# Kernel optimization log

Measured on AMD Instinct MI355X. Metric: run time of the kernel, lower is better.

## Reference

```python
import jax, jax.numpy as jnp
import numpy as np

NUM_HEAD = 16
EMB_DIM = 1024
HEAD_DIM = EMB_DIM // NUM_HEAD

def setup_inputs() -> dict:
    key = jax.random.key(0)
    ks = jax.random.split(key, 9)
    B, S, D = 2, 2048, EMB_DIM
    s = 1.0 / np.sqrt(D)
    return {
        "x": jax.random.normal(ks[0], (B, S, D), dtype=jnp.float32),
        "Wq": jax.random.normal(ks[1], (D, D), dtype=jnp.float32) * s,
        "bq": jnp.zeros((D,), dtype=jnp.float32),
        "Wk": jax.random.normal(ks[2], (D, D), dtype=jnp.float32) * s,
        "bk": jnp.zeros((D,), dtype=jnp.float32),
        "Wv": jax.random.normal(ks[3], (D, D), dtype=jnp.float32) * s,
        "bv": jnp.zeros((D,), dtype=jnp.float32),
        "Wo": jax.random.normal(ks[4], (D, D), dtype=jnp.float32) * s,
        "bo": jnp.zeros((D,), dtype=jnp.float32),
    }

def reference(x, Wq, bq, Wk, bk, Wv, bv, Wo, bo):
    B, S, D = x.shape
    H, Hd = NUM_HEAD, HEAD_DIM
    # projections (torch Linear: x @ W.T + b; here W stored as [in, out])
    Q = (x @ Wq + bq).reshape(B, S, H, Hd)
    K = (x @ Wk + bk).reshape(B, S, H, Hd)
    V = (x @ Wv + bv).reshape(B, S, H, Hd)
    scale = jnp.sqrt(jnp.asarray(Hd, dtype=x.dtype))
    scores = jnp.einsum('bqhd,bkhd->bhqk', Q, K) / scale  # [B,H,S,S]
    attn = jax.nn.softmax(scores, axis=-1)
    out = jnp.einsum('bhql,blhd->bqhd', attn, V).reshape(B, S, D)
    return out @ Wo + bo
```

## Files before the change

### kernel.cpp

```cpp
#include <hip/hip_runtime.h>
#include <math.h>


using bf16   = __bf16;
using bf16x8 = __attribute__((ext_vector_type(8))) __bf16;
using bf16x4 = __attribute__((ext_vector_type(4))) __bf16;
using f32x4  = __attribute__((ext_vector_type(4))) float;

#define MFMA16(a, b, c) __builtin_amdgcn_mfma_f32_16x16x32_bf16((a), (b), (c), 0, 0, 0)
#define WAIT_VM0() asm volatile("s_waitcnt vmcnt(0)" ::: "memory")
#define WAITBAR(N) asm volatile("s_waitcnt vmcnt(" #N ")\n\ts_barrier" ::: "memory")

__device__ __forceinline__ bf16x8 ld8(const bf16* p) { return *(const bf16x8*)p; }

__device__ __forceinline__ void ldg_lds16(bf16* lds_base, const bf16* g) {
    __builtin_amdgcn_global_load_lds(
        (const __attribute__((address_space(1))) void*)g,
        (__attribute__((address_space(3))) void*)lds_base, 16, 0, 0);
}

__device__ __forceinline__ float fast_exp2(float x) {
#if __has_builtin(__builtin_amdgcn_exp2f)
    return __builtin_amdgcn_exp2f(x);
#else
    return exp2f(x);
#endif
}

__global__ __launch_bounds__(256) void prep_kernel(
    const float* __restrict__ x, const float* __restrict__ Wq,
    const float* __restrict__ Wk, const float* __restrict__ Wv,
    const float* __restrict__ Wo, bf16* __restrict__ xb,
    bf16* __restrict__ WtBase) {
    const int z = blockIdx.z;
    const int tid = threadIdx.x;
    if (z == 4) {
        int id = blockIdx.y * 32 + blockIdx.x;
#pragma unroll
        for (int k = 0; k < 4; ++k) {
            int i = id * 4096 + k * 1024 + tid * 4;
            float4 v = *(const float4*)&x[i];
            bf16x4 o = { (bf16)v.x, (bf16)v.y, (bf16)v.z, (bf16)v.w };
            *(bf16x4*)&xb[i] = o;
        }
        return;
    }
    __shared__ float tile[32][33];
    const float* W = (z == 0) ? Wq : (z == 1) ? Wk : (z == 2) ? Wv : Wo;
    bf16* Wt = WtBase + (size_t)z * 1024 * 1024;
    const int tx = tid & 31, ty = tid >> 5;
    const int x0 = blockIdx.x * 32, y0 = blockIdx.y * 32;
#pragma unroll
    for (int i = 0; i < 4; ++i)
        tile[ty + i * 8][tx] = W[(size_t)(y0 + ty + i * 8) * 1024 + x0 + tx];
    __syncthreads();
#pragma unroll
    for (int i = 0; i < 4; ++i)
        Wt[(size_t)(x0 + ty + i * 8) * 1024 + y0 + tx] = (bf16)tile[tx][ty + i * 8];
}

__device__ __forceinline__ void gemm_stage(const bf16* __restrict__ src, int r0,
                                           int k0, bf16* dst, int w, int lane) {
#pragma unroll
    for (int c = 0; c < 2; ++c) {
        int flat = (w * 2 + c) * 64 + lane;
        int row = flat >> 2, cc = flat & 3;
        int gk = (cc ^ ((row >> 1) & 3)) * 8;
        ldg_lds16(dst + (size_t)(w * 2 + c) * 512,
                  src + (size_t)(r0 + row) * 1024 + k0 + gk);
    }
}

__device__ __forceinline__ void gemm_core_128(const bf16* __restrict__ A,
                                              const bf16* __restrict__ Bt,
                                              int m0, int n0,
                                              bf16* As, bf16* Bs,
                                              f32x4 (&acc)[4][4]) {
    const int tid = threadIdx.x, lane = tid & 63, w = tid >> 6;
    const int lo = lane & 15, quad = lane >> 4;
    const int wm = w >> 1, wn = w & 1;

    gemm_stage(A,  m0, 0, As, w, lane);
    gemm_stage(Bt, n0, 0, Bs, w, lane);
    WAIT_VM0();
    __syncthreads();

    for (int it = 0; it < 32; ++it) {
        const int buf = it & 1;
        if (it + 1 < 32) {
            gemm_stage(A,  m0, (it + 1) * 32, As + (buf ^ 1) * 4096, w, lane);
            gemm_stage(Bt, n0, (it + 1) * 32, Bs + (buf ^ 1) * 4096, w, lane);
        }
        const bf16* Ab = As + buf * 4096;
        const bf16* Bb = Bs + buf * 4096;
        bf16x8 af[4], bq[4];
#pragma unroll
        for (int t = 0; t < 4; ++t) {
            int r = wm * 64 + t * 16 + lo;
            af[t] = ld8(&Ab[r * 32 + ((quad ^ ((r >> 1) & 3)) * 8)]);
        }
#pragma unroll
        for (int t = 0; t < 4; ++t) {
            int r = wn * 64 + t * 16 + lo;
            bq[t] = ld8(&Bb[r * 32 + ((quad ^ ((r >> 1) & 3)) * 8)]);
        }
#pragma unroll
        for (int mt = 0; mt < 4; ++mt)
#pragma unroll
            for (int nt = 0; nt < 4; ++nt)
                acc[mt][nt] = MFMA16(af[mt], bq[nt], acc[mt][nt]);
        WAIT_VM0();
        __syncthreads();
    }
}

__global__ __launch_bounds__(256, 3) void qkv_gemm_kernel(
    const bf16* __restrict__ Xb, const bf16* __restrict__ Wts,
    const float* __restrict__ bq, const float* __restrict__ bk,
    const float* __restrict__ bv,
    bf16* __restrict__ Qo, bf16* __restrict__ Ko, bf16* __restrict__ Vto) {
    __shared__ bf16 Smem[4 * 4096];
    bf16* As = Smem;
    bf16* Bs = Smem + 2 * 4096;
    const int z = blockIdx.z;
    const bf16*  Bt   = Wts + (size_t)z * 1024 * 1024;
    const float* bias = (z == 0) ? bq : (z == 1) ? bk : bv;
    const int m0 = blockIdx.y * 128, n0 = blockIdx.x * 128;

    f32x4 acc[4][4] = {};
    gemm_core_128(Xb, Bt, m0, n0, As, Bs, acc);

    const int tid = threadIdx.x;
    const int lane = tid & 63, w = tid >> 6;
    const int lo = lane & 15, quad = lane >> 4;
    const int wm = w >> 1, wn = w & 1;
    const float QSCALE = 0.125f * 1.44269504088896f;

    if (z == 2) {
        bf16* T = Smem;
        const int b = m0 >> 11;
        const int s_base = m0 & 2047;
#pragma unroll
        for (int half = 0; half < 2; ++half) {
            __syncthreads();
            if (wm == half) {
#pragma unroll
                for (int nt = 0; nt < 4; ++nt)
#pragma unroll
                    for (int mt = 0; mt < 4; ++mt)
#pragma unroll
                        for (int r = 0; r < 4; ++r) {
                            int nn = wn * 64 + nt * 16 + lo;
                            int mm = mt * 16 + quad * 4 + r;
                            T[nn * 68 + mm] = (bf16)(acc[mt][nt][r] + bias[n0 + nn]);
                        }
            }
            __syncthreads();
#pragma unroll
            for (int p = 0; p < 8; ++p) {
                int pos = p * 1024 + tid * 4;
                int row = pos >> 6, col = pos & 63;
                int n = n0 + row, h = n >> 6, hd = n & 63;
                int colp = (col & 32) | (((col >> 2) & 3) << 3)
                         | (((col >> 4) & 1) << 2) | (col & 3);
                bf16x4 v = *(const bf16x4*)&T[row * 68 + col];
                *(bf16x4*)&Vto[((size_t)((b * 16 + h) * 64 + hd) << 11)
                               + s_base + half * 64 + colp] = v;
            }
        }
    } else {
#pragma unroll
        for (int mt = 0; mt < 4; ++mt)
#pragma unroll
            for (int nt = 0; nt < 4; ++nt)
#pragma unroll
                for (int r = 0; r < 4; ++r) {
                    int m = m0 + wm * 64 + mt * 16 + quad * 4 + r;
                    int n = n0 + wn * 64 + nt * 16 + lo;
                    float v = acc[mt][nt][r] + bias[n];
                    int b = m >> 11, s = m & 2047, h = n >> 6, hd = n & 63;
                    if (z == 0)
                        Qo[((size_t)((b * 16 + h) * 2048 + s) << 6) + hd] = (bf16)(v * QSCALE);
                    else
                        Ko[((size_t)((b * 16 + h) * 2048 + s) << 6) + hd] = (bf16)v;
                }
    }
}

__global__ __launch_bounds__(256, 2) void out_gemm_kernel(
    const bf16* __restrict__ A, const bf16* __restrict__ Bt,
    const float* __restrict__ bo, float* __restrict__ Co) {
    __shared__ bf16 As[2 * 2048];
    __shared__ bf16 Bs[2 * 4096];
    const int tid = threadIdx.x, lane = tid & 63, w = tid >> 6;
    const int lo = lane & 15, quad = lane >> 4;
    const int wm = w >> 1, wn = w & 1;
    const int m0 = blockIdx.y * 64, n0 = blockIdx.x * 128;

    auto stageA = [&](int k0, bf16* dst) {
        int flat = w * 64 + lane;
        int row = flat >> 2, cc = flat & 3;
        int gk = (cc ^ ((row >> 1) & 3)) * 8;
        ldg_lds16(dst + (size_t)w * 512, A + (size_t)(m0 + row) * 1024 + k0 + gk);
    };
    auto stageB = [&](int k0, bf16* dst) {
#pragma unroll
        for (int c = 0; c < 2; ++c) {
            int flat = (w * 2 + c) * 64 + lane;
            int row = flat >> 2, cc = flat & 3;
            int gk = (cc ^ ((row >> 1) & 3)) * 8;
            ldg_lds16(dst + (size_t)(w * 2 + c) * 512,
                      Bt + (size_t)(n0 + row) * 1024 + k0 + gk);
        }
    };

    f32x4 acc[2][4] = {};
    stageA(0, As);
    stageB(0, Bs);
    WAIT_VM0();
    __syncthreads();

    for (int it = 0; it < 32; ++it) {
        const int buf = it & 1;
        if (it + 1 < 32) {
            stageA((it + 1) * 32, As + (buf ^ 1) * 2048);
            stageB((it + 1) * 32, Bs + (buf ^ 1) * 4096);
        }
        const bf16* Ab = As + buf * 2048;
        const bf16* Bb = Bs + buf * 4096;
        bf16x8 af[2], bq[4];
#pragma unroll
        for (int t = 0; t < 2; ++t) {
            int r = wm * 32 + t * 16 + lo;
            af[t] = ld8(&Ab[r * 32 + ((quad ^ ((r >> 1) & 3)) * 8)]);
        }
#pragma unroll
        for (int t = 0; t < 4; ++t) {
            int r = wn * 64 + t * 16 + lo;
            bq[t] = ld8(&Bb[r * 32 + ((quad ^ ((r >> 1) & 3)) * 8)]);
        }
#pragma unroll
        for (int mt = 0; mt < 2; ++mt)
#pragma unroll
            for (int nt = 0; nt < 4; ++nt)
                acc[mt][nt] = MFMA16(af[mt], bq[nt], acc[mt][nt]);
        WAIT_VM0();
        __syncthreads();
    }

#pragma unroll
    for (int mt = 0; mt < 2; ++mt)
#pragma unroll
        for (int nt = 0; nt < 4; ++nt)
#pragma unroll
            for (int r = 0; r < 4; ++r) {
                int m = m0 + wm * 32 + mt * 16 + quad * 4 + r;
                int n = n0 + wn * 64 + nt * 16 + lo;
                Co[(size_t)m * 1024 + n] = acc[mt][nt][r] + bo[n];
            }
}

__global__ __launch_bounds__(256, 2) void attn_kernel(
    const bf16* __restrict__ Q, const bf16* __restrict__ K,
    const bf16* __restrict__ Vt, bf16* __restrict__ AO) {
    __shared__ bf16 Ks[4][64 * 64];
    __shared__ bf16 Vs[4][64 * 64];
    const int tid = threadIdx.x, w = tid >> 6, lane = tid & 63;
    const int lo = lane & 15, quad = lane >> 4;
    const int blk = blockIdx.x;
    const int bh = (blk & 7) | ((blk >> 7) << 3);
    const int qb = (blk >> 3) & 15;
    const int q0 = qb * 128 + w * 32;

    const bf16* Qb = Q + ((size_t)bh * 2048 + q0) * 64;
    const bf16* Kb = K + (size_t)bh * 2048 * 64;
    const bf16* Vb = Vt + (size_t)bh * 64 * 2048;

    bf16x8 qa[2][2];
#pragma unroll
    for (int qt = 0; qt < 2; ++qt)
#pragma unroll
        for (int ks = 0; ks < 2; ++ks)
            qa[qt][ks] = ld8(&Qb[(qt * 16 + lo) * 64 + ks * 32 + quad * 8]);

    f32x4 O[2][4] = {};
    float l_acc[2] = { 0.f, 0.f };
    const f32x4 ZERO = { 0.f, 0.f, 0.f, 0.f };

    auto stage = [&](int s0, int buf) {
#pragma unroll
        for (int c = 0; c < 2; ++c) {
            int flat = (w * 2 + c) * 64 + lane;
            int row = flat >> 3, cc = flat & 7;
            int g = (cc ^ (row & 7)) * 8;
            ldg_lds16(&Ks[buf][(w * 2 + c) * 512], &Kb[(size_t)(s0 + row) * 64 + g]);
            ldg_lds16(&Vs[buf][(w * 2 + c) * 512], &Vb[(size_t)row * 2048 + s0 + g]);
        }
    };

    const int swz = lo & 7;

    auto qk = [&](int nb, f32x4 (&S)[2][4]) {
        const bf16* Kt = &Ks[nb][0];
#pragma unroll
        for (int t = 0; t < 4; ++t) {
            int r = t * 16 + lo;
            bf16x8 kf0 = ld8(&Kt[r * 64 + ((quad ^ swz) * 8)]);
            S[0][t] = MFMA16(kf0, qa[0][0], ZERO);
            S[1][t] = MFMA16(kf0, qa[1][0], ZERO);
            bf16x8 kf1 = ld8(&Kt[r * 64 + (((quad + 4) ^ swz) * 8)]);
            S[0][t] = MFMA16(kf1, qa[0][1], S[0][t]);
            S[1][t] = MFMA16(kf1, qa[1][1], S[1][t]);
        }
    };

    auto expP = [&](f32x4 (&Sin)[2][4], bf16x8 (&pa)[2][2]) {
#pragma unroll
        for (int qt = 0; qt < 2; ++qt)
#pragma unroll
            for (int kc = 0; kc < 2; ++kc) {
                float e0 = fast_exp2(Sin[qt][2 * kc][0]);
                float e1 = fast_exp2(Sin[qt][2 * kc][1]);
                float e2 = fast_exp2(Sin[qt][2 * kc][2]);
                float e3 = fast_exp2(Sin[qt][2 * kc][3]);
                float e4 = fast_exp2(Sin[qt][2 * kc + 1][0]);
                float e5 = fast_exp2(Sin[qt][2 * kc + 1][1]);
                float e6 = fast_exp2(Sin[qt][2 * kc + 1][2]);
                float e7 = fast_exp2(Sin[qt][2 * kc + 1][3]);
                l_acc[qt] += ((e0 + e1) + (e2 + e3)) + ((e4 + e5) + (e6 + e7));
                pa[qt][kc] = bf16x8{ (bf16)e0, (bf16)e1, (bf16)e2, (bf16)e3,
                                     (bf16)e4, (bf16)e5, (bf16)e6, (bf16)e7 };
            }
    };

    auto pv = [&](int cb, bf16x8 (&pa)[2][2]) {
        const bf16* Vl = &Vs[cb][0];
#pragma unroll
        for (int kc = 0; kc < 2; ++kc)
#pragma unroll
            for (int nt = 0; nt < 4; ++nt) {
                int r = nt * 16 + lo;
                bf16x8 vf = ld8(&Vl[r * 64 + ((((kc * 4 + quad) ^ swz)) * 8)]);
                O[0][nt] = MFMA16(pa[0][kc], vf, O[0][nt]);
                O[1][nt] = MFMA16(pa[1][kc], vf, O[1][nt]);
            }
    };

    auto step = [&](f32x4 (&Sin)[2][4], f32x4 (&Sout)[2][4], int cb, int nb) {
        bf16x8 pa[2][2];
        expP(Sin, pa);
        qk(nb, Sout);
        pv(cb, pa);
    };

    stage(0, 0);
    stage(64, 1);
    WAITBAR(4);

    f32x4 Sa[2][4], Sb[2][4];
    qk(0, Sa);

    for (int it = 0; it < 30; it += 2) {
        stage((it + 2) * 64, (it + 2) & 3);
        WAITBAR(4);
        step(Sa, Sb, it & 3, (it + 1) & 3);
        stage((it + 3) * 64, (it + 3) & 3);
        WAITBAR(4);
        step(Sb, Sa, (it + 1) & 3, (it + 2) & 3);
    }
    WAITBAR(0);
    step(Sa, Sb, 2, 3);
    {
        bf16x8 pa[2][2];
        expP(Sb, pa);
        pv(3, pa);
    }

    const int bb = bh >> 4, h = bh & 15;
#pragma unroll
    for (int qt = 0; qt < 2; ++qt) {
        float lt = l_acc[qt];
        lt += __shfl_xor(lt, 16, 64);
        lt += __shfl_xor(lt, 32, 64);
        const size_t outbase = ((size_t)(bb * 2048 + q0 + qt * 16)) * 1024 + h * 64;
#pragma unroll
        for (int r = 0; r < 4; ++r) {
            float rl = 1.0f / __shfl(lt, quad * 4 + r, 64);
            size_t rowoff = outbase + (size_t)(quad * 4 + r) * 1024;
#pragma unroll
            for (int nt = 0; nt < 4; ++nt)
                AO[rowoff + nt * 16 + lo] = (bf16)(O[qt][nt][r] * rl);
        }
    }
}

extern "C" void kernel_launch(void* const* d_in, const int* in_sizes, int n_in,
                              void* d_out, int out_size, void* d_ws, size_t ws_size,
                              hipStream_t stream) {
    const float* x  = (const float*)d_in[0];
    const float* Wq = (const float*)d_in[1];
    const float* bq = (const float*)d_in[2];
    const float* Wk = (const float*)d_in[3];
    const float* bk = (const float*)d_in[4];
    const float* Wv = (const float*)d_in[5];
    const float* bv = (const float*)d_in[6];
    const float* Wo = (const float*)d_in[7];
    const float* bo = (const float*)d_in[8];
    float* out = (float*)d_out;

    bf16* wsb = (bf16*)d_ws;
    const size_t M1 = 1024u * 1024u;
    bf16* Xb  = wsb;
    bf16* AO  = wsb;
    bf16* Wt  = wsb + 4 * M1;
    bf16* Qw  = wsb + 8 * M1;
    bf16* Kw  = wsb + 12 * M1;
    bf16* Vtw = wsb + 16 * M1;

    prep_kernel<<<dim3(32, 32, 5), 256, 0, stream>>>(x, Wq, Wk, Wv, Wo, Xb, Wt);
    qkv_gemm_kernel<<<dim3(8, 32, 3), 256, 0, stream>>>(Xb, Wt, bq, bk, bv, Qw, Kw, Vtw);
    attn_kernel<<<512, 256, 0, stream>>>(Qw, Kw, Vtw, AO);
    out_gemm_kernel<<<dim3(8, 64), 256, 0, stream>>>(AO, Wt + 3 * M1, bo, out);
}
```

Before: 179.7 us.

## Enlarge QKV GEMM tiles to 256x256 with 8 waves and 4-stage pipeline

The QKV projection GEMM now uses 256x256 output tiles with 512 threads (2x4 waves, each computing 128x64). The shared-memory pipeline goes from double-buffered to a 4-deep ring with prefetch distance 2, using partial vmcnt waits in place of a full drain each iteration. This raises data reuse per loaded tile and hides more global latency. In exchange it uses more LDS and registers per block and launches fewer blocks (192 vs 768), which may underfill the GPU's compute units.

```diff
diff --git a/kernel.cpp b/kernel.cpp
--- a/kernel.cpp
+++ b/kernel.cpp
@@ -71,111 +71,102 @@
     }
 }
 
-__device__ __forceinline__ void gemm_core_128(const bf16* __restrict__ A,
-                                              const bf16* __restrict__ Bt,
-                                              int m0, int n0,
-                                              bf16* As, bf16* Bs,
-                                              f32x4 (&acc)[4][4]) {
-    const int tid = threadIdx.x, lane = tid & 63, w = tid >> 6;
-    const int lo = lane & 15, quad = lane >> 4;
-    const int wm = w >> 1, wn = w & 1;
-
-    gemm_stage(A,  m0, 0, As, w, lane);
-    gemm_stage(Bt, n0, 0, Bs, w, lane);
-    WAIT_VM0();
-    __syncthreads();
-
-    for (int it = 0; it < 32; ++it) {
-        const int buf = it & 1;
-        if (it + 1 < 32) {
-            gemm_stage(A,  m0, (it + 1) * 32, As + (buf ^ 1) * 4096, w, lane);
-            gemm_stage(Bt, n0, (it + 1) * 32, Bs + (buf ^ 1) * 4096, w, lane);
-        }
-        const bf16* Ab = As + buf * 4096;
-        const bf16* Bb = Bs + buf * 4096;
-        bf16x8 af[4], bq[4];
-#pragma unroll
-        for (int t = 0; t < 4; ++t) {
-            int r = wm * 64 + t * 16 + lo;
-            af[t] = ld8(&Ab[r * 32 + ((quad ^ ((r >> 1) & 3)) * 8)]);
-        }
-#pragma unroll
-        for (int t = 0; t < 4; ++t) {
-            int r = wn * 64 + t * 16 + lo;
-            bq[t] = ld8(&Bb[r * 32 + ((quad ^ ((r >> 1) & 3)) * 8)]);
-        }
-#pragma unroll
-        for (int mt = 0; mt < 4; ++mt)
-#pragma unroll
-            for (int nt = 0; nt < 4; ++nt)
-                acc[mt][nt] = MFMA16(af[mt], bq[nt], acc[mt][nt]);
-        WAIT_VM0();
-        __syncthreads();
-    }
-}
-
-__global__ __launch_bounds__(256, 3) void qkv_gemm_kernel(
+__global__ __launch_bounds__(512, 2) void qkv_gemm_kernel(
     const bf16* __restrict__ Xb, const bf16* __restrict__ Wts,
     const float* __restrict__ bq, const float* __restrict__ bk,
     const float* __restrict__ bv,
     bf16* __restrict__ Qo, bf16* __restrict__ Ko, bf16* __restrict__ Vto) {
-    __shared__ bf16 Smem[4 * 4096];
-    bf16* As = Smem;
-    bf16* Bs = Smem + 2 * 4096;
+    __shared__ bf16 As[4 * 8192];
+    __shared__ bf16 Bs[4 * 8192];
     const int z = blockIdx.z;
     const bf16*  Bt   = Wts + (size_t)z * 1024 * 1024;
     const float* bias = (z == 0) ? bq : (z == 1) ? bk : bv;
-    const int m0 = blockIdx.y * 128, n0 = blockIdx.x * 128;
-
-    f32x4 acc[4][4] = {};
-    gemm_core_128(Xb, Bt, m0, n0, As, Bs, acc);
-
-    const int tid = threadIdx.x;
-    const int lane = tid & 63, w = tid >> 6;
+    const int m0 = blockIdx.y * 256, n0 = blockIdx.x * 256;
+    const int tid = threadIdx.x, lane = tid & 63, w = tid >> 6;
     const int lo = lane & 15, quad = lane >> 4;
-    const int wm = w >> 1, wn = w & 1;
+    const int wm = w >> 2, wn = w & 3;
+
+    f32x4 acc[8][4] = {};
+
+    gemm_stage(Xb, m0, 0, As, w, lane);
+    gemm_stage(Bt, n0, 0, Bs, w, lane);
+    gemm_stage(Xb, m0, 32, As + 8192, w, lane);
+    gemm_stage(Bt, n0, 32, Bs + 8192, w, lane);
+
+    int rbuf = 0, sbuf = 2;
+    for (int it = 0; it < 32; ++it) {
+        if (it < 31) { WAITBAR(4); } else { WAITBAR(0); }
+        if (it + 2 < 32) {
+            gemm_stage(Xb, m0, (it + 2) * 32, As + sbuf * 8192, w, lane);
+            gemm_stage(Bt, n0, (it + 2) * 32, Bs + sbuf * 8192, w, lane);
+            sbuf = (sbuf + 1) & 3;
+        }
+        const bf16* Ab = As + rbuf * 8192;
+        const bf16* Bb = Bs + rbuf * 8192;
+        bf16x8 af[8], bf[4];
+#pragma unroll
+        for (int t = 0; t < 8; ++t) {
+            int r = wm * 128 + t * 16 + lo;
+            af[t] = ld8(&Ab[r * 32 + ((quad ^ ((r >> 1) & 3)) * 8)]);
+        }
+#pragma unroll
+        for (int t = 0; t < 4; ++t) {
+            int r = wn * 64 + t * 16 + lo;
+            bf[t] = ld8(&Bb[r * 32 + ((quad ^ ((r >> 1) & 3)) * 8)]);
+        }
+#pragma unroll
+        for (int mt = 0; mt < 8; ++mt)
+#pragma unroll
+            for (int nt = 0; nt < 4; ++nt)
+                acc[mt][nt] = MFMA16(af[mt], bf[nt], acc[mt][nt]);
+        rbuf = (rbuf + 1) & 3;
+    }
+
     const float QSCALE = 0.125f * 1.44269504088896f;
 
     if (z == 2) {
-        bf16* T = Smem;
+        bf16* T = As;
         const int b = m0 >> 11;
-        const int s_base = m0 & 2047;
-#pragma unroll
-        for (int half = 0; half < 2; ++half) {
+        const int c0 = (m0 & 2047) >> 6;
+#pragma unroll
+        for (int hm = 0; hm < 4; ++hm) {
             __syncthreads();
-            if (wm == half) {
+            if (wm == (hm >> 1)) {
+                const int mfb = (hm & 1) * 4;
 #pragma unroll
                 for (int nt = 0; nt < 4; ++nt)
 #pragma unroll
-                    for (int mt = 0; mt < 4; ++mt)
+                    for (int mf = 0; mf < 4; ++mf)
 #pragma unroll
                         for (int r = 0; r < 4; ++r) {
                             int nn = wn * 64 + nt * 16 + lo;
-                            int mm = mt * 16 + quad * 4 + r;
-                            T[nn * 68 + mm] = (bf16)(acc[mt][nt][r] + bias[n0 + nn]);
+                            int mm = mf * 16 + quad * 4 + r;
+                            T[nn * 68 + mm] =
+                                (bf16)(acc[mfb + mf][nt][r] + bias[n0 + nn]);
                         }
             }
             __syncthreads();
+            const int c = c0 + hm;
 #pragma unroll
             for (int p = 0; p < 8; ++p) {
-                int pos = p * 1024 + tid * 4;
+                int pos = p * 2048 + tid * 4;
                 int row = pos >> 6, col = pos & 63;
                 int n = n0 + row, h = n >> 6, hd = n & 63;
                 int colp = (col & 32) | (((col >> 2) & 3) << 3)
                          | (((col >> 4) & 1) << 2) | (col & 3);
                 bf16x4 v = *(const bf16x4*)&T[row * 68 + col];
                 *(bf16x4*)&Vto[((size_t)((b * 16 + h) * 64 + hd) << 11)
-                               + s_base + half * 64 + colp] = v;
+                               + c * 64 + colp] = v;
             }
         }
     } else {
 #pragma unroll
-        for (int mt = 0; mt < 4; ++mt)
+        for (int mt = 0; mt < 8; ++mt)
 #pragma unroll
             for (int nt = 0; nt < 4; ++nt)
 #pragma unroll
                 for (int r = 0; r < 4; ++r) {
-                    int m = m0 + wm * 64 + mt * 16 + quad * 4 + r;
+                    int m = m0 + wm * 128 + mt * 16 + quad * 4 + r;
                     int n = n0 + wn * 64 + nt * 16 + lo;
                     float v = acc[mt][nt][r] + bias[n];
                     int b = m >> 11, s = m & 2047, h = n >> 6, hd = n & 63;
@@ -418,7 +409,7 @@
     bf16* Vtw = wsb + 16 * M1;
 
     prep_kernel<<<dim3(32, 32, 5), 256, 0, stream>>>(x, Wq, Wk, Wv, Wo, Xb, Wt);
-    qkv_gemm_kernel<<<dim3(8, 32, 3), 256, 0, stream>>>(Xb, Wt, bq, bk, bv, Qw, Kw, Vtw);
+    qkv_gemm_kernel<<<dim3(4, 16, 3), 512, 0, stream>>>(Xb, Wt, bq, bk, bv, Qw, Kw, Vtw);
     attn_kernel<<<512, 256, 0, stream>>>(Qw, Kw, Vtw, AO);
     out_gemm_kernel<<<dim3(8, 64), 256, 0, stream>>>(AO, Wt + 3 * M1, bo, out);
 }
```

Result: slower. 192.1 us (+6.9%).
